# Performance work log

Measured on AMD Instinct MI355X. Metric: run time of the kernel, lower is better.

## Reference

```python
import jax, jax.numpy as jnp
import numpy as np

B, R, T, N = 64, 2, 32, 128
C_IN, C_OUT = 64, 64
PRELU_INIT = 0.25


def setup_inputs() -> dict:
    key = jax.random.key(0)
    ks = jax.random.split(key, 6)
    x = jax.random.normal(ks[0], (B, C_IN, T, N), dtype=jnp.float32)
    A = jax.random.uniform(ks[1], (B, R, T, N, N), dtype=jnp.float32)  # non-negative adjacency
    # per-relation 1x1 conv (t_kernel_size=1, relation=1 per gcn since split=[])
    w_gcn = jax.random.normal(ks[2], (R, C_OUT, C_IN), dtype=jnp.float32) * (1.0 / np.sqrt(C_IN))
    b_gcn = jnp.zeros((R, C_OUT), dtype=jnp.float32)
    # tcn temporal conv: kernel (3,1), padding (1,0)
    w_tcn = jax.random.normal(ks[3], (C_OUT, C_OUT, 3, 1), dtype=jnp.float32) * (1.0 / np.sqrt(3 * C_OUT))
    b_tcn = jnp.zeros((C_OUT,), dtype=jnp.float32)
    a_tcn = jnp.float32(PRELU_INIT)  # PReLU inside tcn
    a_out = jnp.float32(PRELU_INIT)  # final PReLU
    return {"x": x, "A": A, "w_gcn": w_gcn, "b_gcn": b_gcn,
            "w_tcn": w_tcn, "b_tcn": b_tcn, "a_tcn": a_tcn, "a_out": a_out}


def _prelu(x, a):
    return jnp.where(x >= 0, x, a * x)


def _normalized_laplacian_tilde(A):
    # A: (..., N, N); A_tilde = A + I, return D^{-1/2} A_tilde D^{-1/2}
    n = A.shape[-1]
    A_t = A + jnp.eye(n, dtype=A.dtype)
    d_inv_sqrt = jax.lax.rsqrt(A_t.sum(-1))  # (..., N); rowsum >= 1
    return d_inv_sqrt[..., :, None] * A_t * d_inv_sqrt[..., None, :]


def reference(x, A, w_gcn, b_gcn, w_tcn, b_tcn, a_tcn, a_out):
    # x: (B,C,T,N), A: (B,R,T,N,N). Eval mode: drop_edge is identity, dropout inactive.
    res = x  # in_channels == out_channels, stride == 1
    # per-relation 1x1 convs, batched over R
    x_c = jnp.einsum('bctn,roc->brotn', x, w_gcn) + b_gcn[None, :, :, None, None]
    A_norm = _normalized_laplacian_tilde(A)  # (B,R,T,N,N)
    # bmm per (r,t): out[b,c,m] = sum_n x_c[b,r,c,t,n] * A_norm[b,r,t,n,m], summed over r
    x_comb = jnp.einsum('brctn,brtnm->bctm', x_c, A_norm)
    # tcn: PReLU -> Conv2d (3,1) pad (1,0) -> Dropout(0)
    h = _prelu(x_comb, a_tcn)
    h = jax.lax.conv_general_dilated(
        h, w_tcn, window_strides=(1, 1), padding=((1, 1), (0, 0)),
        dimension_numbers=('NCHW', 'OIHW', 'NCHW'))
    h = h + b_tcn[None, :, None, None]
    out = _prelu(h + res, a_out)
    return (out, A)
```

## Files before the change

### kernel.cpp

```cpp
#include <hip/hip_runtime.h>
#include <hip/hip_bf16.h>

typedef unsigned short u16;
typedef unsigned int u32;
typedef __attribute__((ext_vector_type(8))) short bf16x8;
typedef __attribute__((ext_vector_type(4))) float f32x4;
typedef __attribute__((ext_vector_type(4))) u16 u16x4;
typedef __attribute__((ext_vector_type(8))) u16 u16x8;

#define B_ 64
#define R_ 2
#define T_ 32
#define N_ 128
#define C_ 64

__device__ __forceinline__ u16 f2bf(float f) {
  return __builtin_bit_cast(u16, __float2bfloat16(f));
}
__device__ __forceinline__ float bf2f(u16 h) {
  u32 u = ((u32)h) << 16;
  return __builtin_bit_cast(float, u);
}

#define MFMA __builtin_amdgcn_mfma_f32_16x16x32_bf16

#define BAR()                                                  \
  do {                                                         \
    asm volatile("s_waitcnt lgkmcnt(0)" ::: "memory");         \
    __builtin_amdgcn_s_barrier();                              \
    __builtin_amdgcn_sched_barrier(0);                         \
  } while (0)

__device__ __forceinline__ void a_load(float4* av, const float* Aslice, int ch, int tid) {
  const int arow = tid >> 2, aseg = tid & 3;
  const float* ap = Aslice + (size_t)(ch * 64 + arow) * N_ + aseg * 32;
#pragma unroll
  for (int j = 0; j < 8; ++j) av[j] = *(const float4*)(ap + 4 * j);
}
__device__ __forceinline__ void a_store(const float4* av, float* Oslice, int ch, int tid) {
  const int arow = tid >> 2, aseg = tid & 3;
  float* op = Oslice + (size_t)(ch * 64 + arow) * N_ + aseg * 32;
#pragma unroll
  for (int j = 0; j < 8; ++j) *(float4*)(op + 4 * j) = av[j];
}

__device__ __forceinline__ void at_write(const float4* av, int ch, int tid,
                                         u16 (*AT)[72], float* dinvr) {
  const int arow = tid >> 2, aseg = tid & 3;
  const int n = ch * 64 + arow;
  float part = 0.f;
#pragma unroll
  for (int j = 0; j < 8; ++j) part += (av[j].x + av[j].y) + (av[j].z + av[j].w);
  part += __shfl_xor(part, 1);
  part += __shfl_xor(part, 2);
  const float d = rsqrtf(part + 1.0f);
  if (aseg == 0) dinvr[n] = d;
  const int col = arow ^ (aseg << 4);
#pragma unroll
  for (int j = 0; j < 8; ++j) {
#pragma unroll
    for (int k = 0; k < 4; ++k) {
      const int m = aseg * 32 + 4 * j + k;
      float v = ((const float*)&av[j])[k];
      if (m == n) v += 1.0f;
      AT[m][col] = f2bf(v * d);
    }
  }
}

__device__ __forceinline__ void load_wg(bf16x8 wf[2][2], const float* wg, int r,
                                        int wr, int lr, int lg) {
#pragma unroll
  for (int kk = 0; kk < 2; ++kk)
#pragma unroll
    for (int mr = 0; mr < 2; ++mr) {
      const float* p = wg + ((size_t)(r * C_ + 32 * wr + 16 * mr + lr)) * C_ + 32 * kk + 8 * lg;
      float4 a = *(const float4*)p, b = *(const float4*)(p + 4);
      bf16x8 f;
      f[0] = (short)f2bf(a.x); f[1] = (short)f2bf(a.y);
      f[2] = (short)f2bf(a.z); f[3] = (short)f2bf(a.w);
      f[4] = (short)f2bf(b.x); f[5] = (short)f2bf(b.y);
      f[6] = (short)f2bf(b.z); f[7] = (short)f2bf(b.w);
      wf[kk][mr] = f;
    }
}

__device__ __forceinline__ void mm1f(u16 (*TMP)[128], const bf16x8 wf[2][2],
                                     const bf16x8 bfr[2][4], const float4 bias[2],
                                     int wr, int wc, int lr, int lg) {
  f32x4 acc1[2][4] = {};
#pragma unroll
  for (int kk = 0; kk < 2; ++kk)
#pragma unroll
    for (int mr = 0; mr < 2; ++mr)
#pragma unroll
      for (int nc = 0; nc < 4; ++nc)
        acc1[mr][nc] = MFMA(wf[kk][mr], bfr[kk][nc], acc1[mr][nc], 0, 0, 0);
#pragma unroll
  for (int mr = 0; mr < 2; ++mr) {
    const int o0 = 32 * wr + 16 * mr + 4 * lg;
    const float bb[4] = {bias[mr].x, bias[mr].y, bias[mr].z, bias[mr].w};
#pragma unroll
    for (int nc = 0; nc < 4; ++nc) {
      const int n = 64 * wc + 16 * nc + lr;
#pragma unroll
      for (int i = 0; i < 4; ++i)
        TMP[o0 + i][n ^ (i << 4)] = f2bf(acc1[mr][nc][i] + bb[i]);
    }
  }
}

__device__ __forceinline__ void mm2_half(f32x4 accr[2][4], const u16 (*TMP)[128],
                                         const u16 (*AT)[72], int ch,
                                         int wr, int wc, int lr, int lg) {
#pragma unroll
  for (int kkin = 0; kkin < 2; ++kkin) {
    bf16x8 af[2], bfr[4];
#pragma unroll
    for (int mr = 0; mr < 2; ++mr) {
      const int c = 32 * wr + 16 * mr + lr;
      const int colT = (ch * 64 + 32 * kkin + 8 * lg) ^ ((lr & 3) << 4);
      af[mr] = *(const bf16x8*)&TMP[c][colT];
    }
#pragma unroll
    for (int nc = 0; nc < 4; ++nc) {
      const int m = 64 * wc + 16 * nc + lr;
      const int colA = (32 * kkin + 8 * lg) ^ (((m >> 5) & 3) << 4);
      bfr[nc] = *(const bf16x8*)&AT[m][colA];
    }
#pragma unroll
    for (int mr = 0; mr < 2; ++mr)
#pragma unroll
      for (int nc = 0; nc < 4; ++nc)
        accr[mr][nc] = MFMA(af[mr], bfr[nc], accr[mr][nc], 0, 0, 0);
  }
}

__device__ __forceinline__ void fold(f32x4 acc2[2][4], f32x4 accr[2][4],
                                     const float* dinvr, int wc, int lr) {
#pragma unroll
  for (int nc = 0; nc < 4; ++nc) {
    const float dm = dinvr[64 * wc + 16 * nc + lr];
#pragma unroll
    for (int mr = 0; mr < 2; ++mr)
#pragma unroll
      for (int i = 0; i < 4; ++i) {
        acc2[mr][nc][i] += dm * accr[mr][nc][i];
        accr[mr][nc][i] = 0.f;
      }
  }
}

__global__ __launch_bounds__(256, 2) void k_gcn(
    const float* __restrict__ x, const float* __restrict__ A,
    const float* __restrict__ wg, const float* __restrict__ bg,
    float* __restrict__ outA, u16* __restrict__ wsX) {
  __shared__ __align__(16) u16 AT[2][N_][72];
  __shared__ __align__(16) u16 TMP[C_][128];
  __shared__ float dinv[R_][N_];

  const int tid = threadIdx.x;
  const int bid = ((blockIdx.x & 7) << 8) | (blockIdx.x >> 3);
  const int b = bid >> 5, t = bid & 31;
  const int lane = tid & 63, wv = tid >> 6;
  const int wr = wv >> 1, wc = wv & 1;
  const int lr = lane & 15, lg = lane >> 4;

  const size_t Asl0 = ((size_t)((b * R_ + 0) * T_ + t)) * (size_t)(N_ * N_);
  const size_t Asl1 = ((size_t)((b * R_ + 1) * T_ + t)) * (size_t)(N_ * N_);

  float4 xv[8];
  {
    const int c = tid & 63, ub = tid >> 6;
    const float* xp = x + ((size_t)(b * C_ + c) * T_ + t) * N_ + 32 * ub;
#pragma unroll
    for (int j = 0; j < 8; ++j) xv[j] = *(const float4*)(xp + 4 * j);
  }
  float4 avA[8], avB[8];
  a_load(avA, A + Asl0, 0, tid);
  a_load(avB, A + Asl0, 1, tid);
  bf16x8 wf0[2][2], wf1[2][2];
  load_wg(wf0, wg, 0, wr, lr, lg);
  load_wg(wf1, wg, 1, wr, lr, lg);
  float4 bias[R_][2];
#pragma unroll
  for (int r = 0; r < R_; ++r)
#pragma unroll
    for (int mr = 0; mr < 2; ++mr)
      bias[r][mr] = *(const float4*)(bg + r * C_ + 32 * wr + 16 * mr + 4 * lg);

  u16 (*XT)[64] = (u16(*)[64])TMP;
  {
    const int c = tid & 63, ub = tid >> 6;
#pragma unroll
    for (int j = 0; j < 8; ++j) {
      const int n0 = 32 * ub + 4 * j;
      XT[n0 + 0][c] = f2bf(xv[j].x);
      XT[n0 + 1][c ^ 16] = f2bf(xv[j].y);
      XT[n0 + 2][c ^ 32] = f2bf(xv[j].z);
      XT[n0 + 3][c ^ 48] = f2bf(xv[j].w);
    }
  }
  BAR();

  bf16x8 bfrx[2][4];
#pragma unroll
  for (int kk = 0; kk < 2; ++kk)
#pragma unroll
    for (int nc = 0; nc < 4; ++nc) {
      const int n = 64 * wc + 16 * nc + lr;
      const int col = (32 * kk + 8 * lg) ^ ((lr & 3) << 4);
      bfrx[kk][nc] = *(const bf16x8*)&XT[n][col];
    }
  BAR();

  mm1f(TMP, wf0, bfrx, bias[0], wr, wc, lr, lg);
  at_write(avA, 0, tid, AT[0], dinv[0]);
  a_store(avA, outA + Asl0, 0, tid);
  BAR();

  f32x4 acc2[2][4] = {};
  f32x4 accr[2][4] = {};

  a_load(avA, A + Asl1, 0, tid);
  mm2_half(accr, TMP, AT[0], 0, wr, wc, lr, lg);
  at_write(avB, 1, tid, AT[1], dinv[0]);
  a_store(avB, outA + Asl0, 1, tid);
  BAR();

  a_load(avB, A + Asl1, 1, tid);
  mm2_half(accr, TMP, AT[1], 1, wr, wc, lr, lg);
  fold(acc2, accr, dinv[0], wc, lr);
  at_write(avA, 0, tid, AT[0], dinv[1]);
  a_store(avA, outA + Asl1, 0, tid);
  BAR();

  mm1f(TMP, wf1, bfrx, bias[1], wr, wc, lr, lg);
  BAR();

  mm2_half(accr, TMP, AT[0], 0, wr, wc, lr, lg);
  at_write(avB, 1, tid, AT[1], dinv[1]);
  a_store(avB, outA + Asl1, 1, tid);
  BAR();

  mm2_half(accr, TMP, AT[1], 1, wr, wc, lr, lg);
  fold(acc2, accr, dinv[1], wc, lr);
  BAR();

  u16* stage = &TMP[0][0];
#pragma unroll
  for (int mr = 0; mr < 2; ++mr)
#pragma unroll
    for (int nc = 0; nc < 4; ++nc) {
      const int m = 64 * wc + 16 * nc + lr;
      const int c0 = 32 * wr + 16 * mr + 4 * lg;
#pragma unroll
      for (int i = 0; i < 4; ++i)
        stage[m * 64 + ((c0 + i) ^ ((m & 7) << 3))] = f2bf(acc2[mr][nc][i]);
    }
  BAR();
  {
    u16* wp = wsX + ((size_t)(b * T_ + t) * N_) * C_;
#pragma unroll
    for (int it = 0; it < 4; ++it) {
      const int idx = it * 2048 + tid * 8;
      const int m = idx >> 6, a = idx & 63;
      u16x8 v = *(const u16x8*)&stage[m * 64 + a];
      *(u16x8*)(wp + m * 64 + (a ^ ((m & 7) << 3))) = v;
    }
  }
}

__global__ __launch_bounds__(256, 3) void k_tcn(
    const u16* __restrict__ wsX, const float* __restrict__ x,
    const float* __restrict__ wt, const float* __restrict__ bt,
    const float* __restrict__ a_tcn, const float* __restrict__ a_out,
    float* __restrict__ out) {
  __shared__ __align__(16) u16 HT[N_][200];
  const int tid = threadIdx.x;
  const int bid = ((blockIdx.x & 7) << 8) | (blockIdx.x >> 3);
  const int b = bid >> 5, t = bid & 31;
  const int lane = tid & 63, wv = tid >> 6;
  const int wr = wv >> 1, wc = wv & 1;
  const int lr = lane & 15, lg = lane >> 4;
  const float at = a_tcn[0], ao = a_out[0];

  bf16x8 wfr[6][2];
#pragma unroll
  for (int kk = 0; kk < 6; ++kk) {
    const int dt = kk >> 1;
    const int ci0 = (32 * kk + 8 * lg) & 63;
#pragma unroll
    for (int mr = 0; mr < 2; ++mr) {
      const int co = 32 * wr + 16 * mr + lr;
      const float* p = wt + ((size_t)co * C_ + ci0) * 3 + dt;
      float e[8];
#pragma unroll
      for (int j = 0; j < 8; ++j) e[j] = p[3 * j];
      bf16x8 f;
#pragma unroll
      for (int j = 0; j < 8; ++j) f[j] = (short)f2bf(e[j]);
      wfr[kk][mr] = f;
    }
  }

#pragma unroll
  for (int dt = 0; dt < 3; ++dt) {
    const int t2 = t + dt - 1;
    const bool ok = (t2 >= 0) && (t2 < T_);
    const u16* p = wsX + ((size_t)(b * T_ + (ok ? t2 : 0)) * N_) * C_;
    u16x4 hv[8];
#pragma unroll
    for (int it = 0; it < 8; ++it) {
      const int idx = it * 256 + tid;
      const int n = idx >> 4, c4 = (idx & 15) * 4;
      u16x4 z = {0, 0, 0, 0};
      hv[it] = ok ? *(const u16x4*)(p + n * C_ + c4) : z;
    }
#pragma unroll
    for (int it = 0; it < 8; ++it) {
      const int idx = it * 256 + tid;
      const int n = idx >> 4, c4 = (idx & 15) * 4;
      u16x4 o;
#pragma unroll
      for (int j = 0; j < 4; ++j) {
        float f = bf2f(hv[it][j]);
        o[j] = f2bf(f < 0.f ? at * f : f);
      }
      *(u16x4*)&HT[n][dt * 64 + c4] = o;
    }
  }
  __syncthreads();

  f32x4 acc[2][4] = {};
#pragma unroll
  for (int kk = 0; kk < 6; ++kk) {
    bf16x8 bfr[4];
#pragma unroll
    for (int nc = 0; nc < 4; ++nc)
      bfr[nc] = *(const bf16x8*)&HT[64 * wc + 16 * nc + lr][32 * kk + 8 * lg];
#pragma unroll
    for (int mr = 0; mr < 2; ++mr)
#pragma unroll
      for (int nc = 0; nc < 4; ++nc)
        acc[mr][nc] = MFMA(wfr[kk][mr], bfr[nc], acc[mr][nc], 0, 0, 0);
  }

#pragma unroll
  for (int mr = 0; mr < 2; ++mr) {
    const int co0 = 32 * wr + 16 * mr + 4 * lg;
    float bts[4];
#pragma unroll
    for (int i = 0; i < 4; ++i) bts[i] = bt[co0 + i];
#pragma unroll
    for (int nc = 0; nc < 4; ++nc) {
      const int n = 64 * wc + 16 * nc + lr;
#pragma unroll
      for (int i = 0; i < 4; ++i) {
        const size_t gi = ((size_t)(b * C_ + co0 + i) * T_ + t) * N_ + n;
        float v = acc[mr][nc][i] + bts[i] + x[gi];
        out[gi] = (v < 0.f) ? ao * v : v;
      }
    }
  }
}

extern "C" void kernel_launch(void* const* d_in, const int* in_sizes, int n_in,
                              void* d_out, int out_size, void* d_ws, size_t ws_size,
                              hipStream_t stream) {
  const float* x = (const float*)d_in[0];
  const float* A = (const float*)d_in[1];
  const float* wg = (const float*)d_in[2];
  const float* bg = (const float*)d_in[3];
  const float* wt = (const float*)d_in[4];
  const float* bt = (const float*)d_in[5];
  const float* atc = (const float*)d_in[6];
  const float* aoc = (const float*)d_in[7];
  float* out = (float*)d_out;
  float* outA = out + (size_t)B_ * C_ * T_ * N_;
  u16* wsX = (u16*)d_ws;

  k_gcn<<<B_ * T_, 256, 0, stream>>>(x, A, wg, bg, outA, wsX);
  k_tcn<<<B_ * T_, 256, 0, stream>>>(wsX, x, wt, bt, atc, aoc, out);
}
```

Baseline: 217.5 us.

## Split A passthrough copy into dedicated copy blocks alongside compute blocks

Doubles the gcn grid and gives half the blocks a copy-only role that streams the A slices to the output, removing the a_store calls from the compute blocks. The compute path is rescheduled with fewer barriers and a deferred load of the second weight set, which lowers register pressure. A is now read twice from global memory, once by the copy blocks and once by the compute blocks, which adds HBM traffic in exchange for freeing the compute blocks from store work.

```diff
diff --git a/kernel.cpp b/kernel.cpp
--- a/kernel.cpp
+++ b/kernel.cpp
@@ -36,12 +36,6 @@
   const float* ap = Aslice + (size_t)(ch * 64 + arow) * N_ + aseg * 32;
 #pragma unroll
   for (int j = 0; j < 8; ++j) av[j] = *(const float4*)(ap + 4 * j);
-}
-__device__ __forceinline__ void a_store(const float4* av, float* Oslice, int ch, int tid) {
-  const int arow = tid >> 2, aseg = tid & 3;
-  float* op = Oslice + (size_t)(ch * 64 + arow) * N_ + aseg * 32;
-#pragma unroll
-  for (int j = 0; j < 8; ++j) *(float4*)(op + 4 * j) = av[j];
 }
 
 __device__ __forceinline__ void at_write(const float4* av, int ch, int tid,
@@ -160,14 +154,38 @@
   __shared__ float dinv[R_][N_];
 
   const int tid = threadIdx.x;
-  const int bid = ((blockIdx.x & 7) << 8) | (blockIdx.x >> 3);
-  const int b = bid >> 5, t = bid & 31;
+  const int raw = blockIdx.x;
+  const int grp = raw >> 4, sub = raw & 15;
+  const int role = sub >> 3;
+  const int pair = (grp << 3) | (sub & 7);
+  const int b = pair >> 5, t = pair & 31;
+
+  const size_t Asl0 = ((size_t)((b * R_ + 0) * T_ + t)) * (size_t)(N_ * N_);
+  const size_t Asl1 = ((size_t)((b * R_ + 1) * T_ + t)) * (size_t)(N_ * N_);
+
+  if (role == 1) {
+#pragma unroll
+    for (int r2 = 0; r2 < R_; ++r2) {
+      const size_t sl = r2 ? Asl1 : Asl0;
+      const float* s = A + sl;
+      float* d = outA + sl;
+#pragma unroll
+      for (int half = 0; half < 2; ++half) {
+        float4 v[8];
+#pragma unroll
+        for (int j = 0; j < 8; ++j)
+          v[j] = *(const float4*)(s + half * 8192 + j * 1024 + tid * 4);
+#pragma unroll
+        for (int j = 0; j < 8; ++j)
+          *(float4*)(d + half * 8192 + j * 1024 + tid * 4) = v[j];
+      }
+    }
+    return;
+  }
+
   const int lane = tid & 63, wv = tid >> 6;
   const int wr = wv >> 1, wc = wv & 1;
   const int lr = lane & 15, lg = lane >> 4;
-
-  const size_t Asl0 = ((size_t)((b * R_ + 0) * T_ + t)) * (size_t)(N_ * N_);
-  const size_t Asl1 = ((size_t)((b * R_ + 1) * T_ + t)) * (size_t)(N_ * N_);
 
   float4 xv[8];
   {
@@ -179,9 +197,8 @@
   float4 avA[8], avB[8];
   a_load(avA, A + Asl0, 0, tid);
   a_load(avB, A + Asl0, 1, tid);
-  bf16x8 wf0[2][2], wf1[2][2];
+  bf16x8 wf0[2][2];
   load_wg(wf0, wg, 0, wr, lr, lg);
-  load_wg(wf1, wg, 1, wr, lr, lg);
   float4 bias[R_][2];
 #pragma unroll
   for (int r = 0; r < R_; ++r)
@@ -214,35 +231,31 @@
     }
   BAR();
 
-  mm1f(TMP, wf0, bfrx, bias[0], wr, wc, lr, lg);
-  at_write(avA, 0, tid, AT[0], dinv[0]);
-  a_store(avA, outA + Asl0, 0, tid);
-  BAR();
-
   f32x4 acc2[2][4] = {};
   f32x4 accr[2][4] = {};
 
+  mm1f(TMP, wf0, bfrx, bias[0], wr, wc, lr, lg);
+  bf16x8 wf1[2][2];
+  load_wg(wf1, wg, 1, wr, lr, lg);
+  at_write(avA, 0, tid, AT[0], dinv[0]);
   a_load(avA, A + Asl1, 0, tid);
+  BAR();
+
   mm2_half(accr, TMP, AT[0], 0, wr, wc, lr, lg);
   at_write(avB, 1, tid, AT[1], dinv[0]);
-  a_store(avB, outA + Asl0, 1, tid);
-  BAR();
-
   a_load(avB, A + Asl1, 1, tid);
+  BAR();
+
   mm2_half(accr, TMP, AT[1], 1, wr, wc, lr, lg);
   fold(acc2, accr, dinv[0], wc, lr);
   at_write(avA, 0, tid, AT[0], dinv[1]);
-  a_store(avA, outA + Asl1, 0, tid);
   BAR();
 
   mm1f(TMP, wf1, bfrx, bias[1], wr, wc, lr, lg);
+  at_write(avB, 1, tid, AT[1], dinv[1]);
   BAR();
 
   mm2_half(accr, TMP, AT[0], 0, wr, wc, lr, lg);
-  at_write(avB, 1, tid, AT[1], dinv[1]);
-  a_store(avB, outA + Asl1, 1, tid);
-  BAR();
-
   mm2_half(accr, TMP, AT[1], 1, wr, wc, lr, lg);
   fold(acc2, accr, dinv[1], wc, lr);
   BAR();
@@ -380,6 +393,6 @@
   float* outA = out + (size_t)B_ * C_ * T_ * N_;
   u16* wsX = (u16*)d_ws;
 
-  k_gcn<<<B_ * T_, 256, 0, stream>>>(x, A, wg, bg, outA, wsX);
+  k_gcn<<<2 * B_ * T_, 256, 0, stream>>>(x, A, wg, bg, outA, wsX);
   k_tcn<<<B_ * T_, 256, 0, stream>>>(wsX, x, wt, bt, atc, aoc, out);
 }
```

Measured after the change: 241.8 us. +11.2%, slower.

## Stream adjacency via async global-to-LDS loads with triple-buffered 32-row chunks

Applied to the files above, without the earlier changes.

Replaces the register-staged adjacency loads with direct global-to-LDS loads into a three-deep ring of 32-row chunks, and interleaves eight chunk consumptions with the MFMA steps under explicit vmcnt waits. The aim is to hide A load latency and cut register pressure. The row degree scaling is applied at the end through two separate per-relation accumulators instead of a fold per relation. Per-node inverse degrees are written to scratch in the output buffer, which k_tcn later overwrites. This adds more barriers and more LDS traffic.

```diff
diff --git a/kernel.cpp b/kernel.cpp
--- a/kernel.cpp
+++ b/kernel.cpp
@@ -24,6 +24,11 @@
 
 #define MFMA __builtin_amdgcn_mfma_f32_16x16x32_bf16
 
+#define STG16(gsrc, ldst)                                                   \
+  __builtin_amdgcn_global_load_lds(                                         \
+      (const __attribute__((address_space(1))) u32*)(gsrc),                 \
+      (__attribute__((address_space(3))) u32*)(ldst), 16, 0, 0)
+
 #define BAR()                                                  \
   do {                                                         \
     asm volatile("s_waitcnt lgkmcnt(0)" ::: "memory");         \
@@ -31,40 +36,58 @@
     __builtin_amdgcn_sched_barrier(0);                         \
   } while (0)
 
-__device__ __forceinline__ void a_load(float4* av, const float* Aslice, int ch, int tid) {
-  const int arow = tid >> 2, aseg = tid & 3;
-  const float* ap = Aslice + (size_t)(ch * 64 + arow) * N_ + aseg * 32;
-#pragma unroll
-  for (int j = 0; j < 8; ++j) av[j] = *(const float4*)(ap + 4 * j);
-}
-__device__ __forceinline__ void a_store(const float4* av, float* Oslice, int ch, int tid) {
-  const int arow = tid >> 2, aseg = tid & 3;
-  float* op = Oslice + (size_t)(ch * 64 + arow) * N_ + aseg * 32;
-#pragma unroll
-  for (int j = 0; j < 8; ++j) *(float4*)(op + 4 * j) = av[j];
-}
-
-__device__ __forceinline__ void at_write(const float4* av, int ch, int tid,
-                                         u16 (*AT)[72], float* dinvr) {
-  const int arow = tid >> 2, aseg = tid & 3;
-  const int n = ch * 64 + arow;
-  float part = 0.f;
-#pragma unroll
-  for (int j = 0; j < 8; ++j) part += (av[j].x + av[j].y) + (av[j].z + av[j].w);
-  part += __shfl_xor(part, 1);
-  part += __shfl_xor(part, 2);
-  const float d = rsqrtf(part + 1.0f);
-  if (aseg == 0) dinvr[n] = d;
-  const int col = arow ^ (aseg << 4);
-#pragma unroll
-  for (int j = 0; j < 8; ++j) {
-#pragma unroll
-    for (int k = 0; k < 4; ++k) {
-      const int m = aseg * 32 + 4 * j + k;
-      float v = ((const float*)&av[j])[k];
-      if (m == n) v += 1.0f;
-      AT[m][col] = f2bf(v * d);
-    }
+#define WAITVM(N)                                              \
+  do {                                                         \
+    asm volatile("s_waitcnt vmcnt(" #N ")" ::: "memory");      \
+    __builtin_amdgcn_sched_barrier(0);                         \
+  } while (0)
+
+__device__ __forceinline__ void gl_chunk(const float* Abase, float* rb,
+                                         int w, int lane) {
+#pragma unroll
+  for (int g = 0; g < 4; ++g) {
+    const int d = (w * 4 + g) * 64 + lane;
+    const int c4 = d >> 5;
+    const int rl = (d & 31) ^ (c4 & 7);
+    STG16(Abase + rl * 128 + c4 * 4, rb + (w * 4 + g) * 256);
+  }
+}
+
+__device__ __forceinline__ void consume(const float* rb, int ch,
+                                        u16 (*ATb)[32], float* outAs,
+                                        float* dscr, int tid, float4* gv) {
+  const int c4 = tid & 31, rb8 = tid >> 5;
+  const float4* rf4 = (const float4*)rb;
+#pragma unroll
+  for (int j = 0; j < 4; ++j)
+    gv[j] = rf4[c4 * 32 + (((rb8 << 2) + j) ^ (c4 & 7))];
+  float d4[4];
+#pragma unroll
+  for (int j = 0; j < 4; ++j) {
+    float s = (gv[j].x + gv[j].y) + (gv[j].z + gv[j].w);
+    s += __shfl_xor(s, 1); s += __shfl_xor(s, 2); s += __shfl_xor(s, 4);
+    s += __shfl_xor(s, 8); s += __shfl_xor(s, 16);
+    d4[j] = rsqrtf(s + 1.0f);
+  }
+  if (c4 == 0) {
+    float4 dv = {d4[0], d4[1], d4[2], d4[3]};
+    *(float4*)(dscr + ch * 32 + rb8 * 4) = dv;
+  }
+#pragma unroll
+  for (int j = 0; j < 4; ++j)
+    *(float4*)(outAs + (size_t)(ch * 32 + rb8 * 4 + j) * N_ + c4 * 4) = gv[j];
+  const int nb = (rb8 << 2) ^ ((c4 & 7) << 2);
+#pragma unroll
+  for (int i = 0; i < 4; ++i) {
+    const int m = c4 * 4 + i;
+    u16x4 pk;
+#pragma unroll
+    for (int j = 0; j < 4; ++j) {
+      float v = ((const float*)&gv[j])[i];
+      if (m == ch * 32 + rb8 * 4 + j) v += 1.0f;
+      pk[j] = f2bf(v * d4[j]);
+    }
+    *(u16x4*)&ATb[m][nb] = pk;
   }
 }
 
@@ -110,64 +133,54 @@
   }
 }
 
-__device__ __forceinline__ void mm2_half(f32x4 accr[2][4], const u16 (*TMP)[128],
-                                         const u16 (*AT)[72], int ch,
-                                         int wr, int wc, int lr, int lg) {
-#pragma unroll
-  for (int kkin = 0; kkin < 2; ++kkin) {
-    bf16x8 af[2], bfr[4];
-#pragma unroll
-    for (int mr = 0; mr < 2; ++mr) {
-      const int c = 32 * wr + 16 * mr + lr;
-      const int colT = (ch * 64 + 32 * kkin + 8 * lg) ^ ((lr & 3) << 4);
-      af[mr] = *(const bf16x8*)&TMP[c][colT];
-    }
-#pragma unroll
-    for (int nc = 0; nc < 4; ++nc) {
-      const int m = 64 * wc + 16 * nc + lr;
-      const int colA = (32 * kkin + 8 * lg) ^ (((m >> 5) & 3) << 4);
-      bfr[nc] = *(const bf16x8*)&AT[m][colA];
-    }
-#pragma unroll
-    for (int mr = 0; mr < 2; ++mr)
-#pragma unroll
-      for (int nc = 0; nc < 4; ++nc)
-        accr[mr][nc] = MFMA(af[mr], bfr[nc], accr[mr][nc], 0, 0, 0);
-  }
-}
-
-__device__ __forceinline__ void fold(f32x4 acc2[2][4], f32x4 accr[2][4],
-                                     const float* dinvr, int wc, int lr) {
+__device__ __forceinline__ void mm2k(f32x4 acc[2][4], const u16 (*TMP)[128],
+                                     const u16 (*ATb)[32], int ch,
+                                     int wr, int wc, int lr, int lg) {
+  bf16x8 af[2], bfr[4];
+#pragma unroll
+  for (int mr = 0; mr < 2; ++mr) {
+    const int c = 32 * wr + 16 * mr + lr;
+    const int colT = (ch * 32 + 8 * lg) ^ ((lr & 3) << 4);
+    af[mr] = *(const bf16x8*)&TMP[c][colT];
+  }
 #pragma unroll
   for (int nc = 0; nc < 4; ++nc) {
-    const float dm = dinvr[64 * wc + 16 * nc + lr];
-#pragma unroll
-    for (int mr = 0; mr < 2; ++mr)
-#pragma unroll
-      for (int i = 0; i < 4; ++i) {
-        acc2[mr][nc][i] += dm * accr[mr][nc][i];
-        accr[mr][nc][i] = 0.f;
-      }
-  }
+    const int m = 64 * wc + 16 * nc + lr;
+    const int swz = ((m >> 2) & 7) << 2;
+    const int base = (8 * lg) ^ (swz & 24);
+    const int s4 = swz & 4;
+    u16x4 h0 = *(const u16x4*)&ATb[m][base + s4];
+    u16x4 h1 = *(const u16x4*)&ATb[m][base + (4 ^ s4)];
+    bf16x8 f;
+    f[0] = (short)h0[0]; f[1] = (short)h0[1]; f[2] = (short)h0[2]; f[3] = (short)h0[3];
+    f[4] = (short)h1[0]; f[5] = (short)h1[1]; f[6] = (short)h1[2]; f[7] = (short)h1[3];
+    bfr[nc] = f;
+  }
+#pragma unroll
+  for (int mr = 0; mr < 2; ++mr)
+#pragma unroll
+    for (int nc = 0; nc < 4; ++nc)
+      acc[mr][nc] = MFMA(af[mr], bfr[nc], acc[mr][nc], 0, 0, 0);
 }
 
 __global__ __launch_bounds__(256, 2) void k_gcn(
     const float* __restrict__ x, const float* __restrict__ A,
     const float* __restrict__ wg, const float* __restrict__ bg,
-    float* __restrict__ outA, u16* __restrict__ wsX) {
-  __shared__ __align__(16) u16 AT[2][N_][72];
+    float* __restrict__ outA, u16* __restrict__ wsX, float* __restrict__ dscrg) {
+  __shared__ __align__(16) float RB[3][32 * 128];
+  __shared__ __align__(16) u16 AT[2][N_][32];
   __shared__ __align__(16) u16 TMP[C_][128];
-  __shared__ float dinv[R_][N_];
 
   const int tid = threadIdx.x;
   const int bid = ((blockIdx.x & 7) << 8) | (blockIdx.x >> 3);
   const int b = bid >> 5, t = bid & 31;
-  const int lane = tid & 63, wv = tid >> 6;
-  const int wr = wv >> 1, wc = wv & 1;
+  const int lane = tid & 63, w = tid >> 6;
+  const int wr = w >> 1, wc = w & 1;
   const int lr = lane & 15, lg = lane >> 4;
 
   const size_t Asl0 = ((size_t)((b * R_ + 0) * T_ + t)) * (size_t)(N_ * N_);
   const size_t Asl1 = ((size_t)((b * R_ + 1) * T_ + t)) * (size_t)(N_ * N_);
+  float* dscr = dscrg + (size_t)bid * 256;
 
   float4 xv[8];
   {
@@ -176,9 +189,6 @@
 #pragma unroll
     for (int j = 0; j < 8; ++j) xv[j] = *(const float4*)(xp + 4 * j);
   }
-  float4 avA[8], avB[8];
-  a_load(avA, A + Asl0, 0, tid);
-  a_load(avB, A + Asl0, 1, tid);
   bf16x8 wf0[2][2], wf1[2][2];
   load_wg(wf0, wg, 0, wr, lr, lg);
   load_wg(wf1, wg, 1, wr, lr, lg);
@@ -188,8 +198,10 @@
 #pragma unroll
     for (int mr = 0; mr < 2; ++mr)
       bias[r][mr] = *(const float4*)(bg + r * C_ + 32 * wr + 16 * mr + 4 * lg);
-
-  u16 (*XT)[64] = (u16(*)[64])TMP;
+  gl_chunk(A + Asl0, RB[0], w, lane);
+  gl_chunk(A + Asl0 + 4096, RB[1], w, lane);
+
+  u16 (*XT)[64] = (u16(*)[64])RB[2];
   {
     const int c = tid & 63, ub = tid >> 6;
 #pragma unroll
@@ -203,6 +215,10 @@
   }
   BAR();
 
+  f32x4 accA[2][4] = {};
+  f32x4 accB[2][4] = {};
+  float4 gvA[4], gvB[4];
+
   bf16x8 bfrx[2][4];
 #pragma unroll
   for (int kk = 0; kk < 2; ++kk)
@@ -212,41 +228,65 @@
       const int col = (32 * kk + 8 * lg) ^ ((lr & 3) << 4);
       bfrx[kk][nc] = *(const bf16x8*)&XT[n][col];
     }
-  BAR();
-
   mm1f(TMP, wf0, bfrx, bias[0], wr, wc, lr, lg);
-  at_write(avA, 0, tid, AT[0], dinv[0]);
-  a_store(avA, outA + Asl0, 0, tid);
-  BAR();
-
-  f32x4 acc2[2][4] = {};
-  f32x4 accr[2][4] = {};
-
-  a_load(avA, A + Asl1, 0, tid);
-  mm2_half(accr, TMP, AT[0], 0, wr, wc, lr, lg);
-  at_write(avB, 1, tid, AT[1], dinv[0]);
-  a_store(avB, outA + Asl0, 1, tid);
-  BAR();
-
-  a_load(avB, A + Asl1, 1, tid);
-  mm2_half(accr, TMP, AT[1], 1, wr, wc, lr, lg);
-  fold(acc2, accr, dinv[0], wc, lr);
-  at_write(avA, 0, tid, AT[0], dinv[1]);
-  a_store(avA, outA + Asl1, 0, tid);
-  BAR();
-
+  WAITVM(4);
+  consume(RB[0], 0, AT[0], outA + Asl0, dscr, tid, gvA);
+  BAR();
+
+  gl_chunk(A + Asl0 + 8192, RB[2], w, lane);
+  mm2k(accA, TMP, AT[0], 0, wr, wc, lr, lg);
+  WAITVM(9);
+  consume(RB[1], 1, AT[1], outA + Asl0, dscr, tid, gvB);
+  BAR();
+
+  gl_chunk(A + Asl0 + 12288, RB[0], w, lane);
+  mm2k(accA, TMP, AT[1], 1, wr, wc, lr, lg);
+  WAITVM(9);
+  consume(RB[2], 2, AT[0], outA + Asl0, dscr, tid, gvA);
+  BAR();
+
+  gl_chunk(A + Asl1, RB[1], w, lane);
+  mm2k(accA, TMP, AT[0], 2, wr, wc, lr, lg);
+  WAITVM(9);
+  consume(RB[0], 3, AT[1], outA + Asl0, dscr, tid, gvB);
+  BAR();
+
+  gl_chunk(A + Asl1 + 4096, RB[2], w, lane);
+  mm2k(accA, TMP, AT[1], 3, wr, wc, lr, lg);
+  WAITVM(9);
+  consume(RB[1], 0, AT[0], outA + Asl1, dscr + 128, tid, gvA);
+  BAR();
+
+  gl_chunk(A + Asl1 + 8192, RB[0], w, lane);
   mm1f(TMP, wf1, bfrx, bias[1], wr, wc, lr, lg);
-  BAR();
-
-  mm2_half(accr, TMP, AT[0], 0, wr, wc, lr, lg);
-  at_write(avB, 1, tid, AT[1], dinv[1]);
-  a_store(avB, outA + Asl1, 1, tid);
-  BAR();
-
-  mm2_half(accr, TMP, AT[1], 1, wr, wc, lr, lg);
-  fold(acc2, accr, dinv[1], wc, lr);
-  BAR();
-
+  WAITVM(9);
+  consume(RB[2], 1, AT[1], outA + Asl1, dscr + 128, tid, gvB);
+  BAR();
+
+  gl_chunk(A + Asl1 + 12288, RB[1], w, lane);
+  mm2k(accB, TMP, AT[0], 0, wr, wc, lr, lg);
+  BAR();
+
+  mm2k(accB, TMP, AT[1], 1, wr, wc, lr, lg);
+  WAITVM(9);
+  consume(RB[0], 2, AT[0], outA + Asl1, dscr + 128, tid, gvA);
+  BAR();
+
+  mm2k(accB, TMP, AT[0], 2, wr, wc, lr, lg);
+  WAITVM(5);
+  consume(RB[1], 3, AT[1], outA + Asl1, dscr + 128, tid, gvB);
+  BAR();
+
+  mm2k(accB, TMP, AT[1], 3, wr, wc, lr, lg);
+  BAR();
+
+  float dA[4], dB[4];
+#pragma unroll
+  for (int nc = 0; nc < 4; ++nc) {
+    const int m = 64 * wc + 16 * nc + lr;
+    dA[nc] = dscr[m];
+    dB[nc] = dscr[128 + m];
+  }
   u16* stage = &TMP[0][0];
 #pragma unroll
   for (int mr = 0; mr < 2; ++mr)
@@ -255,8 +295,10 @@
       const int m = 64 * wc + 16 * nc + lr;
       const int c0 = 32 * wr + 16 * mr + 4 * lg;
 #pragma unroll
-      for (int i = 0; i < 4; ++i)
-        stage[m * 64 + ((c0 + i) ^ ((m & 7) << 3))] = f2bf(acc2[mr][nc][i]);
+      for (int i = 0; i < 4; ++i) {
+        const float v = dA[nc] * accA[mr][nc][i] + dB[nc] * accB[mr][nc][i];
+        stage[m * 64 + ((c0 + i) ^ ((m & 7) << 3))] = f2bf(v);
+      }
     }
   BAR();
   {
@@ -287,9 +329,9 @@
 
   bf16x8 wfr[6][2];
 #pragma unroll
-  for (int kk = 0; kk < 6; ++kk) {
-    const int dt = kk >> 1;
-    const int ci0 = (32 * kk + 8 * lg) & 63;
+  for (int kq = 0; kq < 6; ++kq) {
+    const int dt = kq >> 1;
+    const int ci0 = (32 * kq + 8 * lg) & 63;
 #pragma unroll
     for (int mr = 0; mr < 2; ++mr) {
       const int co = 32 * wr + 16 * mr + lr;
@@ -300,7 +342,7 @@
       bf16x8 f;
 #pragma unroll
       for (int j = 0; j < 8; ++j) f[j] = (short)f2bf(e[j]);
-      wfr[kk][mr] = f;
+      wfr[kq][mr] = f;
     }
   }
 
@@ -311,20 +353,20 @@
     const u16* p = wsX + ((size_t)(b * T_ + (ok ? t2 : 0)) * N_) * C_;
     u16x4 hv[8];
 #pragma unroll
-    for (int it = 0; it < 8; ++it) {
-      const int idx = it * 256 + tid;
+    for (int i3 = 0; i3 < 8; ++i3) {
+      const int idx = i3 * 256 + tid;
       const int n = idx >> 4, c4 = (idx & 15) * 4;
       u16x4 z = {0, 0, 0, 0};
-      hv[it] = ok ? *(const u16x4*)(p + n * C_ + c4) : z;
-    }
-#pragma unroll
-    for (int it = 0; it < 8; ++it) {
-      const int idx = it * 256 + tid;
+      hv[i3] = ok ? *(const u16x4*)(p + n * C_ + c4) : z;
+    }
+#pragma unroll
+    for (int i3 = 0; i3 < 8; ++i3) {
+      const int idx = i3 * 256 + tid;
       const int n = idx >> 4, c4 = (idx & 15) * 4;
       u16x4 o;
 #pragma unroll
       for (int j = 0; j < 4; ++j) {
-        float f = bf2f(hv[it][j]);
+        float f = bf2f(hv[i3][j]);
         o[j] = f2bf(f < 0.f ? at * f : f);
       }
       *(u16x4*)&HT[n][dt * 64 + c4] = o;
@@ -334,16 +376,16 @@
 
   f32x4 acc[2][4] = {};
 #pragma unroll
-  for (int kk = 0; kk < 6; ++kk) {
+  for (int kq = 0; kq < 6; ++kq) {
     bf16x8 bfr[4];
 #pragma unroll
     for (int nc = 0; nc < 4; ++nc)
-      bfr[nc] = *(const bf16x8*)&HT[64 * wc + 16 * nc + lr][32 * kk + 8 * lg];
+      bfr[nc] = *(const bf16x8*)&HT[64 * wc + 16 * nc + lr][32 * kq + 8 * lg];
 #pragma unroll
     for (int mr = 0; mr < 2; ++mr)
 #pragma unroll
       for (int nc = 0; nc < 4; ++nc)
-        acc[mr][nc] = MFMA(wfr[kk][mr], bfr[nc], acc[mr][nc], 0, 0, 0);
+        acc[mr][nc] = MFMA(wfr[kq][mr], bfr[nc], acc[mr][nc], 0, 0, 0);
   }
 
 #pragma unroll
@@ -379,7 +421,8 @@
   float* out = (float*)d_out;
   float* outA = out + (size_t)B_ * C_ * T_ * N_;
   u16* wsX = (u16*)d_ws;
-
-  k_gcn<<<B_ * T_, 256, 0, stream>>>(x, A, wg, bg, outA, wsX);
+  float* dscr = out;
+
+  k_gcn<<<B_ * T_, 256, 0, stream>>>(x, A, wg, bg, outA, wsX, dscr);
   k_tcn<<<B_ * T_, 256, 0, stream>>>(wsX, x, wt, bt, atc, aoc, out);
 }
```

New measurement: 208.7 us. 1.04x faster.
